# Kernel optimization log

Hardware: AMD Instinct MI355X
Metric: run time of the kernel (lower is better)

The kernel has to match this reference:

```python
import jax, jax.numpy as jnp
import numpy as np
from jax import lax

# ---- model dims (match init_kwargs) ----
D = 2048        # hidden_size
HD = 128        # head_dim
HQ = 16         # num_q_heads (= expanded_num_heads)
HK = 8          # num_k_heads = num_v_heads
CONV = 4        # conv_size
CHUNK = 64      # chunk_size
NUM_ITER = 30   # chebyshev iterations
RIDGE = 0.02
EPS = 1e-6


def setup_inputs() -> dict:
    key = jax.random.key(0)
    ks = jax.random.split(key, 20)
    s = 0.02
    inp = {}
    inp['hidden_states'] = jax.random.normal(ks[0], (1, 1024, D), jnp.float32)
    inp['Wq'] = jax.random.normal(ks[1], (D, HQ * HD), jnp.float32) * s
    inp['Wk'] = jax.random.normal(ks[2], (D, HK * HD), jnp.float32) * s
    inp['Wv'] = jax.random.normal(ks[3], (D, HK * HD), jnp.float32) * s
    inp['conv_q'] = jax.random.normal(ks[4], (HQ * HD, CONV), jnp.float32) * 0.3
    inp['conv_k'] = jax.random.normal(ks[5], (HK * HD, CONV), jnp.float32) * 0.3
    inp['conv_v'] = jax.random.normal(ks[6], (HK * HD, CONV), jnp.float32) * 0.3
    inp['Wa'] = jax.random.normal(ks[7], (D, HQ), jnp.float32) * s
    # A_log = log(Uniform(0,16)) as in torch init
    inp['A_log'] = jnp.log(jax.random.uniform(ks[8], (HQ,), jnp.float32, 1e-3, 16.0))
    # dt_bias = inverse-softplus of dt ~ LogUniform(1e-3, 1e-1)
    dt = jnp.exp(jax.random.uniform(ks[9], (HQ,), jnp.float32) * (np.log(0.1) - np.log(0.001)) + np.log(0.001))
    dt = jnp.clip(dt, 1e-4, None)
    inp['dt_bias'] = dt + jnp.log(-jnp.expm1(-dt))
    inp['Wb'] = jax.random.normal(ks[10], (D, HQ), jnp.float32) * s
    inp['bb'] = jnp.zeros((HQ,), jnp.float32)
    inp['Walpha'] = jax.random.normal(ks[11], (D, HQ), jnp.float32) * s
    inp['balpha'] = jnp.zeros((HQ,), jnp.float32)
    inp['Wg'] = jax.random.normal(ks[12], (D, HQ * HD), jnp.float32) * s
    inp['norm_w'] = jnp.ones((HD,), jnp.float32)
    inp['Wo'] = jax.random.normal(ks[13], (HQ * HD, D), jnp.float32) * s
    return inp


def short_conv(x, w):
    # causal depthwise conv1d (kernel=CONV) + silu; x:[B,L,C], w:[C,K]
    K = w.shape[1]
    L = x.shape[1]
    xp = jnp.pad(x, ((0, 0), (K - 1, 0), (0, 0)))
    y = sum(xp[:, j:j + L, :] * w[:, j] for j in range(K))
    return jax.nn.silu(y)


def cheb_solve(A, b, lmin, lmax, num_iter):
    # Chebyshev semi-iteration for SPD A x = b, eigenvalue bounds [lmin, lmax].
    # A, b: [..., d, d]; lmin scalar; lmax: [..., 1, 1]
    theta = (lmax + lmin) / 2.0
    delta = (lmax - lmin) / 2.0
    sigma1 = theta / delta
    x = jnp.zeros_like(b)
    r = b
    rho = 1.0 / sigma1
    dvec = r / theta
    def body(carry, _):
        x, r, dvec, rho = carry
        x = x + dvec
        r = r - jnp.einsum('...de,...ef->...df', A, dvec)
        rho_n = 1.0 / (2.0 * sigma1 - rho)
        dvec = rho_n * rho * dvec + (2.0 * rho_n / delta) * r
        return (x, r, dvec, rho_n), None
    (x, _, _, _), _ = lax.scan(body, (x, r, dvec, rho), None, length=num_iter)
    return x


def reference(hidden_states, Wq, Wk, Wv, conv_q, conv_k, conv_v, Wa, A_log, dt_bias,
              Wb, bb, Walpha, balpha, Wg, norm_w, Wo):
    x = hidden_states
    B, L, _ = x.shape
    H, Hk, d, C = HQ, HK, HD, CHUNK
    Nc = L // C

    # projections + short causal convs with silu
    q = short_conv(x @ Wq, conv_q).reshape(B, L, H, d) * (d ** -0.5)  # gla rescale
    k = short_conv(x @ Wk, conv_k).reshape(B, L, Hk, d)
    v = short_conv(x @ Wv, conv_v).reshape(B, L, Hk, d)
    grp = H // Hk
    k = jnp.repeat(k, grp, axis=2)  # GQA expand: (h g) ordering
    v = jnp.repeat(v, grp, axis=2)

    # gates
    glog = -jnp.exp(A_log) * jax.nn.softplus(x @ Wa + dt_bias)   # [B,L,H], log forgetting gate <= 0
    beta = jax.nn.sigmoid(x @ Wb + bb)                           # [B,L,H]
    alpha = jax.nn.sigmoid(x @ Walpha + balpha)                  # [B,L,H]

    # chunk: [B,H,Nc,C,...]
    def ch(t):
        return t.reshape(B, Nc, C, H, -1).transpose(0, 3, 1, 2, 4)
    qc, kc, vc = ch(q), ch(k), ch(v)
    glc = glog.reshape(B, Nc, C, H).transpose(0, 3, 1, 2)   # [B,H,Nc,C]
    bc = beta.reshape(B, Nc, C, H).transpose(0, 3, 1, 2)

    cs = jnp.cumsum(glc, axis=-1)         # inclusive cumulative log-decay within chunk
    G = cs[..., -1]                        # total chunk decay [B,H,Nc]
    w_end = jnp.exp(G[..., None] - cs) * bc
    dHn = jnp.einsum('bhnc,bhncd,bhnce->bhnde', w_end, kc, kc)  # gram increment (forgetting_gate_kk)
    dBn = jnp.einsum('bhnc,bhncd,bhnce->bhnde', w_end, kc, vc)  # kv increment
    dg = jnp.exp(G)

    # inter-chunk state recurrence (scan over chunks)
    def step(carry, inp):
        Hs, Bs = carry
        g_n, dH_n, dB_n = inp
        out = (Hs, Bs)  # state at chunk START
        Hs = g_n[..., None, None] * Hs + dH_n
        Bs = g_n[..., None, None] * Bs + dB_n
        return (Hs, Bs), out
    init = (jnp.zeros((B, H, d, d), x.dtype), jnp.zeros((B, H, d, d), x.dtype))
    inputs = (dg.transpose(2, 0, 1), dHn.transpose(2, 0, 1, 3, 4), dBn.transpose(2, 0, 1, 3, 4))
    _, (H0, B0) = lax.scan(step, init, inputs)  # [Nc,B,H,d,d]

    # ridge-regularized Kalman solve per chunk via Chebyshev
    A = H0 + RIDGE * jnp.eye(d, dtype=x.dtype)
    lmax = jnp.trace(A, axis1=-2, axis2=-1)[..., None, None]  # trace >= lambda_max for SPD
    X = cheb_solve(A, B0, RIDGE, lmax, NUM_ITER)              # [Nc,B,H,d,d]
    Xc = X.transpose(1, 2, 0, 3, 4)                           # [B,H,Nc,d,d]

    # inter-chunk readout (through solved state)
    o_inter = jnp.exp(cs)[..., None] * jnp.einsum('bhncd,bhnde->bhnce', qc, Xc)
    # intra-chunk causal gated attention
    diff = cs[..., :, None] - cs[..., None, :]                # [B,H,Nc,C,C]
    mask = jnp.tril(jnp.ones((C, C), bool))
    dmat = jnp.exp(jnp.where(mask, diff, -1e30))
    scores = jnp.einsum('bhncd,bhnjd->bhncj', qc, kc) * dmat * bc[..., None, :]
    o_intra = jnp.einsum('bhncj,bhnjd->bhncd', scores, vc)

    o = (o_inter + o_intra).transpose(0, 2, 3, 1, 4).reshape(B, L, H, d)
    o = o + alpha[..., None] * v   # alpha connection (residual value path)

    # gated RMSNorm + output projection
    g_out = (x @ Wg).reshape(B, L, H, d)
    o = o * lax.rsqrt(jnp.mean(o * o, axis=-1, keepdims=True) + EPS) * norm_w
    o = o * jax.nn.silu(g_out)
    return o.reshape(B, L, H * d) @ Wo
```

## Files before the change

### kernel.cpp

```cpp
#include <hip/hip_runtime.h>
#include <math.h>


#define LSEQ 1024
#define DM   2048
#define NHQ  16
#define NHK  8
#define HDIM 128
#define NCH  16
#define CSZ  64

typedef __attribute__((ext_vector_type(8))) short short8;
typedef __attribute__((ext_vector_type(4))) float floatx4;

__device__ __forceinline__ unsigned short f2bf(float f) {
  unsigned int u = __float_as_uint(f);
  u += 0x7fffu + ((u >> 16) & 1u);
  return (unsigned short)(u >> 16);
}
__device__ __forceinline__ float bf2f(unsigned short u) {
  return __uint_as_float(((unsigned int)u) << 16);
}

__device__ __forceinline__ void tcast_body(
    const float* __restrict__ W, unsigned short* __restrict__ Wt,
    int K, int N, int bn, int bk, int tid, float* __restrict__ t) {
  int r = tid >> 5, c = tid & 31;
#pragma unroll
  for (int i = 0; i < 4; ++i)
    t[(r + i * 8) * 33 + c] = W[(size_t)(bk * 32 + r + i * 8) * N + bn * 32 + c];
  __syncthreads();
#pragma unroll
  for (int i = 0; i < 4; ++i)
    Wt[(size_t)(bn * 32 + r + i * 8) * K + bk * 32 + c] =
        f2bf(t[c * 33 + r + i * 8]);
}

__global__ __launch_bounds__(256) void prep_kernel(
    const float* __restrict__ x, const float* __restrict__ Wq,
    const float* __restrict__ Wk, const float* __restrict__ Wv,
    const float* __restrict__ Wg, unsigned short* __restrict__ xb16,
    unsigned short* __restrict__ WtAll) {
  __shared__ float t[32 * 33];
  int b = blockIdx.x, tid = threadIdx.x;
  if (b < 2048) {
    int i = b * 256 + tid;
    float4 v = ((const float4*)x)[i];
    ushort4 u;
    u.x = f2bf(v.x); u.y = f2bf(v.y); u.z = f2bf(v.z); u.w = f2bf(v.w);
    ((ushort4*)xb16)[i] = u;
  } else if (b < 6144) {
    int r = b - 2048;
    tcast_body(Wq, WtAll, 2048, 2048, r & 63, r >> 6, tid, t);
  } else if (b < 8192) {
    int r = b - 6144;
    tcast_body(Wk, WtAll + (size_t)2048 * 2048, 2048, 1024, r & 31, r >> 5, tid, t);
  } else if (b < 10240) {
    int r = b - 8192;
    tcast_body(Wv, WtAll + (size_t)3072 * 2048, 2048, 1024, r & 31, r >> 5, tid, t);
  } else {
    int r = b - 10240;
    tcast_body(Wg, WtAll + (size_t)4096 * 2048, 2048, 2048, r & 63, r >> 6, tid, t);
  }
}

__global__ __launch_bounds__(256) void gemm_bf16(
    const unsigned short* __restrict__ A, const unsigned short* __restrict__ Bt,
    float* __restrict__ C, int M, int N, int K) {
  __shared__ unsigned short As[128 * 72];
  __shared__ unsigned short Bs[64 * 72];
  int tid = threadIdx.x;
  int wave = tid >> 6, lane = tid & 63;
  int ln = lane & 15, hi = lane >> 4;
  int wm = wave & 1, wn = wave >> 1;
  int m0 = blockIdx.y * 128, n0 = blockIdx.x * 64;

  floatx4 acc[4][2];
#pragma unroll
  for (int mt = 0; mt < 4; ++mt)
#pragma unroll
    for (int nt = 0; nt < 2; ++nt) acc[mt][nt] = (floatx4)(0.f);

  for (int k0 = 0; k0 < K; k0 += 64) {
#pragma unroll
    for (int g = 0; g < 4; ++g) {
      int l = tid + g * 256;
      int m = l >> 3, go = l & 7;
      uint4 v = *(const uint4*)(A + (size_t)(m0 + m) * K + k0 + go * 8);
      *(uint4*)(As + m * 72 + go * 8) = v;
    }
#pragma unroll
    for (int g = 0; g < 2; ++g) {
      int l = tid + g * 256;
      int n = l >> 3, go = l & 7;
      uint4 v = *(const uint4*)(Bt + (size_t)(n0 + n) * K + k0 + go * 8);
      *(uint4*)(Bs + n * 72 + go * 8) = v;
    }
    __syncthreads();
#pragma unroll
    for (int kb = 0; kb < 2; ++kb) {
      short8 a[4], b[2];
#pragma unroll
      for (int mt = 0; mt < 4; ++mt)
        a[mt] = *(const short8*)(As + (wm * 64 + mt * 16 + ln) * 72 + kb * 32 + hi * 8);
#pragma unroll
      for (int nt = 0; nt < 2; ++nt)
        b[nt] = *(const short8*)(Bs + (wn * 32 + nt * 16 + ln) * 72 + kb * 32 + hi * 8);
#pragma unroll
      for (int mt = 0; mt < 4; ++mt)
#pragma unroll
        for (int nt = 0; nt < 2; ++nt)
          acc[mt][nt] = __builtin_amdgcn_mfma_f32_16x16x32_bf16(
              a[mt], b[nt], acc[mt][nt], 0, 0, 0);
    }
    __syncthreads();
  }
#pragma unroll
  for (int mt = 0; mt < 4; ++mt)
#pragma unroll
    for (int nt = 0; nt < 2; ++nt) {
      int col = n0 + wn * 32 + nt * 16 + ln;
      int rowb = m0 + wm * 64 + mt * 16 + hi * 4;
#pragma unroll
      for (int r = 0; r < 4; ++r)
        C[(size_t)(rowb + r) * N + col] = acc[mt][nt][r];
    }
}

__device__ __forceinline__ float conv_core(
    const float* __restrict__ xin, const float* __restrict__ w,
    int idx, int instride, int nch, float scale) {
  int t = idx / nch, ch = idx - t * nch;
  float acc = 0.f;
#pragma unroll
  for (int j = 0; j < 4; ++j) {
    int tt = t + j - 3;
    float xv = (tt >= 0) ? xin[(size_t)tt * instride + ch] : 0.f;
    acc = fmaf(xv, w[ch * 4 + j], acc);
  }
  return acc / (1.f + expf(-acc)) * scale;
}

__global__ __launch_bounds__(256) void conv_all(
    const float* __restrict__ xall, const float* __restrict__ convq,
    const float* __restrict__ convk, const float* __restrict__ convv,
    unsigned short* __restrict__ qs16, float* __restrict__ ks2,
    unsigned short* __restrict__ ks16, float* __restrict__ vs2) {
  int b = blockIdx.x, tid = threadIdx.x;
  if (b < 8192) {
    int idx = b * 256 + tid;
    qs16[idx] = f2bf(conv_core(xall, convq, idx, 6144, 2048,
                               0.08838834764831845f));
  } else if (b < 12288) {
    int idx = (b - 8192) * 256 + tid;
    float v = conv_core(xall + 2048, convk, idx, 6144, 1024, 1.0f);
    ks2[idx] = v;
    ks16[idx] = f2bf(v);
  } else {
    int idx = (b - 12288) * 256 + tid;
    vs2[idx] = conv_core(xall + 3072, convv, idx, 6144, 1024, 1.0f);
  }
}

__global__ __launch_bounds__(256) void vtr_kernel(
    const float* __restrict__ vs, unsigned short* __restrict__ vT16) {
  int b = blockIdx.x;
  __shared__ float t[64 * 132];
  int tid = threadIdx.x;
  size_t gbase = ((size_t)(b >> 3)) * 65536 + ((size_t)(b & 7)) * 128;
#pragma unroll
  for (int g = 0; g < 8; ++g) {
    int i = tid + g * 256;
    int c = i >> 5, e4 = i & 31;
    float4 v = *(const float4*)(vs + gbase + (size_t)c * 1024 + e4 * 4);
    t[c * 132 + e4 * 4 + 0] = v.x;
    t[c * 132 + e4 * 4 + 1] = v.y;
    t[c * 132 + e4 * 4 + 2] = v.z;
    t[c * 132 + e4 * 4 + 3] = v.w;
  }
  __syncthreads();
  int e = tid >> 1, half = tid & 1;
  size_t obase = ((size_t)b << 13) + (size_t)e * 64 + half * 32;
#pragma unroll
  for (int cc = 0; cc < 8; ++cc) {
    int c0 = half * 32 + cc * 4;
    ushort4 u;
    u.x = f2bf(t[(c0 + 0) * 132 + e]);
    u.y = f2bf(t[(c0 + 1) * 132 + e]);
    u.z = f2bf(t[(c0 + 2) * 132 + e]);
    u.w = f2bf(t[(c0 + 3) * 132 + e]);
    *(ushort4*)(vT16 + obase + cc * 4) = u;
  }
}

__global__ __launch_bounds__(256) void gates_fused(
    const float* __restrict__ x, const float* __restrict__ Wa,
    const float* __restrict__ Wb, const float* __restrict__ Wal,
    const float* __restrict__ A_log, const float* __restrict__ dtb,
    const float* __restrict__ bbv, const float* __restrict__ balv,
    float* __restrict__ glog, float* __restrict__ beta,
    float* __restrict__ alpha) {
  int t = blockIdx.x;
  __shared__ float xr[2048];
  __shared__ float part[256];
  int tid = threadIdx.x;
  for (int i = tid; i < 512; i += 256)
    ((float4*)xr)[i] = ((const float4*)(x + (size_t)t * 2048))[i];
  __syncthreads();
  int o = tid >> 2, p = tid & 3;
  float s = 0.f;
  if (o < 48) {
    const float* W = (o < 16) ? Wa : (o < 32) ? Wb : Wal;
    int h = o & 15;
    int k0 = p * 512;
    for (int k = k0; k < k0 + 512; ++k) s = fmaf(xr[k], W[k * 16 + h], s);
  }
  part[tid] = s;
  __syncthreads();
  if (o < 48 && p == 0) {
    float dot = part[tid] + part[tid + 1] + part[tid + 2] + part[tid + 3];
    int h = o & 15;
    if (o < 16) {
      float za = dot + dtb[h];
      float sp = fmaxf(za, 0.f) + log1pf(expf(-fabsf(za)));
      glog[t * 16 + h] = -expf(A_log[h]) * sp;
    } else if (o < 32) {
      beta[t * 16 + h] = 1.f / (1.f + expf(-(dot + bbv[h])));
    } else {
      alpha[t * 16 + h] = 1.f / (1.f + expf(-(dot + balv[h])));
    }
  }
}

__global__ __launch_bounds__(256) void cumsum_kernel(
    const float* __restrict__ glog, const float* __restrict__ beta,
    float* __restrict__ cs, float* __restrict__ wend) {
  int idx = threadIdx.x;
  int n = idx & 15;
  float acc = 0.f;
  for (int c = 0; c < CSZ; ++c) {
    acc += glog[(n * CSZ + c) * NHQ + (idx >> 4)];
    cs[idx * CSZ + c] = acc;
  }
  float G = acc;
  for (int c = 0; c < CSZ; ++c) {
    wend[idx * CSZ + c] =
        expf(G - cs[idx * CSZ + c]) * beta[(n * CSZ + c) * NHQ + (idx >> 4)];
  }
}

__global__ __launch_bounds__(256) void dhb_kernel(
    const float* __restrict__ ks, const float* __restrict__ vs,
    const float* __restrict__ wend, float* __restrict__ dH,
    float* __restrict__ dB) {
  int bid = blockIdx.x;
  int h = bid >> 4, n = bid & 15;
  int hk = h >> 1;
  __shared__ unsigned short skF[2][8192];
  __shared__ unsigned short svF[2][8192];
  int tid = threadIdx.x;

#pragma unroll
  for (int p = 0; p < 4; ++p) {
    int t2 = tid + p * 256;
    int c0 = (t2 >> 7) << 3;
    int e = t2 & 127;
    int base = ((e >> 4) * 2 + (c0 >> 5)) * 512 +
               ((c0 & 31) >> 3) * 128 + (e & 15) * 8;
    unsigned short kh[8], kl[8], vh[8], vl[8];
#pragma unroll
    for (int j = 0; j < 8; ++j) {
      int c = c0 + j;
      float s = sqrtf(wend[bid * 64 + c]);
      size_t g = (size_t)(n * 64 + c) * 1024 + hk * 128 + e;
      float kf = s * ks[g];
      float vf = s * vs[g];
      unsigned short khh = f2bf(kf);
      kh[j] = khh; kl[j] = f2bf(kf - bf2f(khh));
      unsigned short vhh = f2bf(vf);
      vh[j] = vhh; vl[j] = f2bf(vf - bf2f(vhh));
    }
    *(uint4*)(&skF[0][base]) = *(uint4*)kh;
    *(uint4*)(&skF[1][base]) = *(uint4*)kl;
    *(uint4*)(&svF[0][base]) = *(uint4*)vh;
    *(uint4*)(&svF[1][base]) = *(uint4*)vl;
  }
  __syncthreads();

  int w = tid >> 6, lane = tid & 63;
  int ln = lane & 15, hi = lane >> 4;

  short8 ah[2][2], al[2][2];
#pragma unroll
  for (int mti = 0; mti < 2; ++mti) {
    int mt = w * 2 + mti;
#pragma unroll
    for (int ct = 0; ct < 2; ++ct) {
      ah[mti][ct] = *(const short8*)(&skF[0][((mt * 2 + ct) * 64 + lane) * 8]);
      al[mti][ct] = *(const short8*)(&skF[1][((mt * 2 + ct) * 64 + lane) * 8]);
    }
  }

  size_t gb = (size_t)bid << 14;
#pragma unroll
  for (int which = 0; which < 2; ++which) {
    const unsigned short (*BF)[8192] = which ? svF : skF;
    float* outp = which ? dB : dH;
#pragma unroll
    for (int nt = 0; nt < 8; ++nt) {
      floatx4 a0 = (floatx4)(0.f), a1 = (floatx4)(0.f);
#pragma unroll
      for (int ct = 0; ct < 2; ++ct) {
        short8 bh = *(const short8*)(&BF[0][((nt * 2 + ct) * 64 + lane) * 8]);
        short8 bl = *(const short8*)(&BF[1][((nt * 2 + ct) * 64 + lane) * 8]);
        a0 = __builtin_amdgcn_mfma_f32_16x16x32_bf16(ah[0][ct], bh, a0, 0, 0, 0);
        a0 = __builtin_amdgcn_mfma_f32_16x16x32_bf16(ah[0][ct], bl, a0, 0, 0, 0);
        a0 = __builtin_amdgcn_mfma_f32_16x16x32_bf16(al[0][ct], bh, a0, 0, 0, 0);
        a1 = __builtin_amdgcn_mfma_f32_16x16x32_bf16(ah[1][ct], bh, a1, 0, 0, 0);
        a1 = __builtin_amdgcn_mfma_f32_16x16x32_bf16(ah[1][ct], bl, a1, 0, 0, 0);
        a1 = __builtin_amdgcn_mfma_f32_16x16x32_bf16(al[1][ct], bh, a1, 0, 0, 0);
      }
      int e = nt * 16 + ln;
#pragma unroll
      for (int rg = 0; rg < 4; ++rg) {
        int d0 = (w * 2 + 0) * 16 + hi * 4 + rg;
        int d1 = (w * 2 + 1) * 16 + hi * 4 + rg;
        outp[gb + (size_t)d0 * 128 + e] = a0[rg];
        outp[gb + (size_t)d1 * 128 + e] = a1[rg];
      }
    }
  }
}

__global__ __launch_bounds__(256) void scan_kernel(
    float* __restrict__ dH, float* __restrict__ dB,
    const float* __restrict__ cs) {
  int idx = blockIdx.x * 256 + threadIdx.x;
  int h = idx >> 14, de = idx & 16383;
  float Hs = 0.f, Bs = 0.f;
  bool diag = ((de % 129) == 0);
#pragma unroll 1
  for (int n = 0; n < NCH; ++n) {
    size_t off = ((size_t)(h * 16 + n) << 14) + de;
    float dh = dH[off], db = dB[off];
    dH[off] = diag ? (Hs + 0.02f) : Hs;
    dB[off] = Bs;
    float g = expf(cs[(h * 16 + n) * CSZ + (CSZ - 1)]);
    Hs = fmaf(g, Hs, dh);
    Bs = fmaf(g, Bs, db);
  }
}

__global__ __launch_bounds__(256) void afrag_kernel(
    float* __restrict__ Aall, float* __restrict__ traces) {
  int bid = blockIdx.x;
  float* Ag = Aall + ((size_t)bid << 14);
  __shared__ float As[16384];
  int tid = threadIdx.x;
  for (int i = tid; i < 4096; i += 256)
    ((float4*)As)[i] = ((const float4*)Ag)[i];
  __syncthreads();
  if (tid < 64) {
    float tv = As[tid * 129] + As[(tid + 64) * 129];
#pragma unroll
    for (int off = 32; off; off >>= 1) tv += __shfl_down(tv, off);
    if (tid == 0) traces[bid] = tv;
  }
  unsigned short* Ah = (unsigned short*)Ag;
  unsigned short* Al = Ah + 16384;
#pragma unroll
  for (int c8 = 0; c8 < 8; ++c8) {
    int s0 = tid * 64 + c8 * 8;
    int frag = s0 >> 9, mlane = (s0 >> 3) & 63;
    int m = ((frag >> 2) << 4) + (mlane & 15);
    int k = ((frag & 3) << 5) + ((mlane >> 4) << 3);
    unsigned short hi[8], lo[8];
#pragma unroll
    for (int j = 0; j < 8; ++j) {
      float a = As[m * 128 + k + j];
      unsigned short h = f2bf(a);
      hi[j] = h;
      lo[j] = f2bf(a - bf2f(h));
    }
    *(uint4*)(Ah + s0) = *(uint4*)hi;
    *(uint4*)(Al + s0) = *(uint4*)lo;
  }
}

__global__ __launch_bounds__(512) void cheb_kernel(
    const unsigned short* __restrict__ Afrag, const float* __restrict__ traces,
    float* __restrict__ Ball) {
  int bid = blockIdx.x;
  const unsigned short* __restrict__ Ah = Afrag + ((size_t)bid << 15);
  float* __restrict__ Bg = Ball + ((size_t)bid << 14);
  __shared__ unsigned short dT[2][16384];
  int tid = threadIdx.x;
  int w = tid >> 6, lane = tid & 63;
  int ln = lane & 15, q = lane >> 4;

  float lmax = traces[bid];
  const float lmin = 0.02f;
  float theta = 0.5f * (lmax + lmin);
  float delta = 0.5f * (lmax - lmin);
  float sigma1 = theta / delta;
  float rho = delta / theta;
  float invtheta = 1.f / theta;

  short8 afr[4][2];
#pragma unroll
  for (int kt = 0; kt < 4; ++kt) {
    afr[kt][0] = *(const short8*)(Ah + (((w * 4 + kt) * 64 + lane) << 3));
    afr[kt][1] = *(const short8*)(Ah + 16384 + (((w * 4 + kt) * 64 + lane) << 3));
  }

  int wrA = ((w >> 1) * 64 + (((w & 1) * 2 + (q >> 1)) * 16 + ln)) * 8 +
            ((q & 1) << 2);

  float xx[8][4], rr[8][4], dd[8][4];
#pragma unroll
  for (int nt = 0; nt < 8; ++nt) {
    int nn = nt * 16 + ln;
    ushort4 pack;
    unsigned short* pp = (unsigned short*)&pack;
#pragma unroll
    for (int rg = 0; rg < 4; ++rg) {
      float b = Bg[(w * 16 + q * 4 + rg) * 128 + nn];
      rr[nt][rg] = b;
      xx[nt][rg] = 0.f;
      unsigned short dq = f2bf(b * invtheta);
      dd[nt][rg] = bf2f(dq);
      pp[rg] = dq;
    }
    *(ushort4*)(&dT[0][nt * 2048 + wrA]) = pack;
  }
  __syncthreads();

#pragma unroll 1
  for (int it = 0; it < 30; ++it) {
    const unsigned short* dTr = dT[it & 1];
    unsigned short* dTw = dT[(it & 1) ^ 1];
    floatx4 acc[8];
#pragma unroll
    for (int nt = 0; nt < 8; ++nt) acc[nt] = (floatx4)(0.f);
#pragma unroll
    for (int kt = 0; kt < 4; ++kt) {
      short8 df[8];
#pragma unroll
      for (int nt = 0; nt < 8; ++nt)
        df[nt] = *(const short8*)(dTr + (((nt * 4 + kt) * 64 + lane) << 3));
#pragma unroll
      for (int nt = 0; nt < 8; ++nt) {
        acc[nt] = __builtin_amdgcn_mfma_f32_16x16x32_bf16(
            afr[kt][0], df[nt], acc[nt], 0, 0, 0);
        acc[nt] = __builtin_amdgcn_mfma_f32_16x16x32_bf16(
            afr[kt][1], df[nt], acc[nt], 0, 0, 0);
      }
    }
    float rho_n = 1.f / (2.f * sigma1 - rho);
    float c1s = rho_n * rho;
    float c2s = 2.f * rho_n / delta;
#pragma unroll
    for (int nt = 0; nt < 8; ++nt) {
      ushort4 pack;
      unsigned short* pp = (unsigned short*)&pack;
#pragma unroll
      for (int rg = 0; rg < 4; ++rg) {
        xx[nt][rg] += dd[nt][rg];
        rr[nt][rg] -= acc[nt][rg];
        float dn = fmaf(c1s, dd[nt][rg], c2s * rr[nt][rg]);
        unsigned short dq = f2bf(dn);
        dd[nt][rg] = bf2f(dq);
        pp[rg] = dq;
      }
      *(ushort4*)(&dTw[nt * 2048 + wrA]) = pack;
    }
    rho = rho_n;
    __syncthreads();
  }

  unsigned short* Xf = (unsigned short*)Bg;
#pragma unroll
  for (int nt = 0; nt < 8; ++nt) {
    ushort4 h4, l4;
    unsigned short* hp = (unsigned short*)&h4;
    unsigned short* lp = (unsigned short*)&l4;
#pragma unroll
    for (int rg = 0; rg < 4; ++rg) {
      float xv = xx[nt][rg];
      unsigned short h = f2bf(xv);
      hp[rg] = h;
      lp[rg] = f2bf(xv - bf2f(h));
    }
    size_t off = (size_t)nt * 2048 + wrA;
    *(ushort4*)(Xf + off) = h4;
    *(ushort4*)(Xf + 16384 + off) = l4;
  }
}

__global__ __launch_bounds__(256) void attn_kernel(
    const unsigned short* __restrict__ q16, const unsigned short* __restrict__ k16,
    const unsigned short* __restrict__ vT16, const unsigned short* __restrict__ Xf,
    const float* __restrict__ vs, const float* __restrict__ cs,
    const float* __restrict__ beta, const float* __restrict__ alpha,
    float* __restrict__ o) {
  int bid = blockIdx.x;
  int h = bid >> 4, n = bid & 15;
  int hk = h >> 1;
  __shared__ unsigned short qb[64 * 136];
  __shared__ unsigned short kb[64 * 136];
  __shared__ unsigned short Sb[64 * 72];
  __shared__ float csL[64], ecsL[64], betaL[64], alphaL[64];
  int tid = threadIdx.x;
  int w = tid >> 6, lane = tid & 63;
  int ln = lane & 15, hi = lane >> 4;

  {
    size_t qgb = (((size_t)(n * 64)) * 16 + h) * 128;
    size_t kgb = (((size_t)(n * 64)) * 8 + hk) * 128;
#pragma unroll
    for (int g = 0; g < 4; ++g) {
      int i = tid + g * 256;
      int c = i >> 4, ch = i & 15;
      *(uint4*)(qb + c * 136 + ch * 8) =
          *(const uint4*)(q16 + qgb + (size_t)c * 2048 + ch * 8);
      *(uint4*)(kb + c * 136 + ch * 8) =
          *(const uint4*)(k16 + kgb + (size_t)c * 1024 + ch * 8);
    }
    if (tid < 64) {
      float cv = cs[bid * 64 + tid];
      csL[tid] = cv;
      ecsL[tid] = expf(cv);
      betaL[tid] = beta[(n * 64 + tid) * 16 + h];
      alphaL[tid] = alpha[(n * 64 + tid) * 16 + h];
    }
  }
  __syncthreads();

  short8 aq[4];
#pragma unroll
  for (int dt = 0; dt < 4; ++dt)
    aq[dt] = *(const short8*)(qb + (w * 16 + ln) * 136 + dt * 32 + hi * 8);

  const unsigned short* Xb = Xf + ((size_t)bid << 15);
  floatx4 acc[8];
#pragma unroll
  for (int et = 0; et < 8; ++et) {
    floatx4 a = (floatx4)(0.f);
#pragma unroll
    for (int dt = 0; dt < 4; ++dt) {
      short8 xh = *(const short8*)(Xb + (et * 4 + dt) * 512 + lane * 8);
      short8 xl = *(const short8*)(Xb + 16384 + (et * 4 + dt) * 512 + lane * 8);
      a = __builtin_amdgcn_mfma_f32_16x16x32_bf16(aq[dt], xh, a, 0, 0, 0);
      a = __builtin_amdgcn_mfma_f32_16x16x32_bf16(aq[dt], xl, a, 0, 0, 0);
    }
    acc[et] = a;
  }
#pragma unroll
  for (int et = 0; et < 8; ++et)
#pragma unroll
    for (int rg = 0; rg < 4; ++rg)
      acc[et][rg] *= ecsL[w * 16 + hi * 4 + rg];

#pragma unroll
  for (int jt = 0; jt < 4; ++jt) {
    if (jt <= w) {
      floatx4 s = (floatx4)(0.f);
#pragma unroll
      for (int dt = 0; dt < 4; ++dt) {
        short8 bk = *(const short8*)(kb + (jt * 16 + ln) * 136 + dt * 32 + hi * 8);
        s = __builtin_amdgcn_mfma_f32_16x16x32_bf16(aq[dt], bk, s, 0, 0, 0);
      }
      int j = jt * 16 + ln;
      float csj = csL[j], bj = betaL[j];
#pragma unroll
      for (int rg = 0; rg < 4; ++rg) {
        int c = w * 16 + hi * 4 + rg;
        float v = (j <= c) ? s[rg] * expf(csL[c] - csj) * bj : 0.f;
        Sb[c * 72 + j] = f2bf(v);
      }
    } else {
#pragma unroll
      for (int rg = 0; rg < 4; ++rg)
        Sb[(w * 16 + hi * 4 + rg) * 72 + jt * 16 + ln] = 0;
    }
  }

  const unsigned short* vTb = vT16 + ((size_t)(n * 8 + hk) << 13);
#pragma unroll
  for (int et = 0; et < 8; ++et) {
#pragma unroll
    for (int kt = 0; kt < 2; ++kt) {
      short8 as = *(const short8*)(Sb + (w * 16 + ln) * 72 + kt * 32 + hi * 8);
      short8 bv = *(const short8*)(vTb + (et * 16 + ln) * 64 + kt * 32 + hi * 8);
      acc[et] = __builtin_amdgcn_mfma_f32_16x16x32_bf16(as, bv, acc[et], 0, 0, 0);
    }
  }

#pragma unroll
  for (int et = 0; et < 8; ++et) {
#pragma unroll
    for (int rg = 0; rg < 4; ++rg) {
      int c = w * 16 + hi * 4 + rg, e = et * 16 + ln;
      size_t oaddr = (((size_t)(n * 64 + c)) * 16 + h) * 128 + e;
      size_t vaddr = (((size_t)(n * 64 + c)) * 8 + hk) * 128 + e;
      o[oaddr] = acc[et][rg] + alphaL[c] * vs[vaddr];
    }
  }
}

__global__ __launch_bounds__(256) void rmso_kernel(
    const float* __restrict__ o, const float* __restrict__ xall,
    const float* __restrict__ norm_w, unsigned short* __restrict__ onorm,
    const float* __restrict__ Wo, unsigned short* __restrict__ WtWo) {
  __shared__ float t[32 * 33];
  int b = blockIdx.x, tid = threadIdx.x;
  if (b < 4096) {
    int wave = tid >> 6, lane = tid & 63;
    int row = b * 4 + wave;
    size_t base = (size_t)row * HDIM;
    size_t gbase = (size_t)(row >> 4) * 6144 + 4096 + (size_t)(row & 15) * HDIM;
    float v0 = o[base + lane], v1 = o[base + lane + 64];
    float ss = fmaf(v0, v0, v1 * v1);
#pragma unroll
    for (int off = 32; off; off >>= 1) ss += __shfl_down(ss, off);
    ss = __shfl(ss, 0);
    float rinv = rsqrtf(ss * (1.f / 128.f) + 1e-6f);
    float g0 = xall[gbase + lane], g1 = xall[gbase + lane + 64];
    float s0 = g0 / (1.f + expf(-g0));
    float s1 = g1 / (1.f + expf(-g1));
    onorm[base + lane]      = f2bf(v0 * rinv * norm_w[lane] * s0);
    onorm[base + lane + 64] = f2bf(v1 * rinv * norm_w[lane + 64] * s1);
  } else {
    int r = b - 4096;
    tcast_body(Wo, WtWo, 2048, 2048, r & 63, r >> 6, tid, t);
  }
}

extern "C" void kernel_launch(void* const* d_in, const int* in_sizes, int n_in,
                              void* d_out, int out_size, void* d_ws,
                              size_t ws_size, hipStream_t stream) {
  (void)in_sizes; (void)n_in; (void)out_size; (void)ws_size;
  const float* x      = (const float*)d_in[0];
  const float* Wq     = (const float*)d_in[1];
  const float* Wk     = (const float*)d_in[2];
  const float* Wv     = (const float*)d_in[3];
  const float* convq  = (const float*)d_in[4];
  const float* convk  = (const float*)d_in[5];
  const float* convv  = (const float*)d_in[6];
  const float* Wa     = (const float*)d_in[7];
  const float* A_log  = (const float*)d_in[8];
  const float* dtb    = (const float*)d_in[9];
  const float* Wb     = (const float*)d_in[10];
  const float* bbv    = (const float*)d_in[11];
  const float* Wal    = (const float*)d_in[12];
  const float* balv   = (const float*)d_in[13];
  const float* Wg     = (const float*)d_in[14];
  const float* norm_w = (const float*)d_in[15];
  const float* Wo     = (const float*)d_in[16];
  float* out = (float*)d_out;

  float* p = (float*)d_ws;
  float* xall  = p; p += 6291456;
  float* qslot = p; p += 2097152;
  float* ks2   = p; p += 1048576;
  float* vs2   = p; p += 1048576;
  float* ob    = p; p += 2097152;
  float* glog  = p; p += 16384;
  float* beta  = p; p += 16384;
  float* alpha = p; p += 16384;
  float* csb   = p; p += 16384;
  float* wend  = p; p += 16384;
  float* traces= p; p += 16384;
  float* dHn   = p; p += 4194304;
  float* dBn   = p; p += 4194304;
  unsigned short* xb16 = (unsigned short*)p; p += 1048576;

  unsigned short* qs16 = (unsigned short*)qslot;
  unsigned short* ks16 = qs16 + 2097152;
  unsigned short* vT16 = ks16 + 1048576;
  unsigned short* WtAll = (unsigned short*)dHn;
  unsigned short* WtWo  = (unsigned short*)ks2;
  unsigned short* onorm16 = xb16;

  dim3 blk(256);
  prep_kernel<<<14336, blk, 0, stream>>>(x, Wq, Wk, Wv, Wg, xb16, WtAll);
  gemm_bf16<<<dim3(96, 8), blk, 0, stream>>>(xb16, WtAll, xall, 1024, 6144, 2048);
  conv_all<<<16384, blk, 0, stream>>>(xall, convq, convk, convv,
                                      qs16, ks2, ks16, vs2);
  vtr_kernel<<<128, blk, 0, stream>>>(vs2, vT16);
  gates_fused<<<1024, blk, 0, stream>>>(x, Wa, Wb, Wal, A_log, dtb, bbv, balv,
                                        glog, beta, alpha);
  cumsum_kernel<<<1, blk, 0, stream>>>(glog, beta, csb, wend);
  dhb_kernel<<<256, blk, 0, stream>>>(ks2, vs2, wend, dHn, dBn);
  scan_kernel<<<1024, blk, 0, stream>>>(dHn, dBn, csb);
  afrag_kernel<<<256, blk, 0, stream>>>(dHn, traces);
  cheb_kernel<<<256, dim3(512), 0, stream>>>((unsigned short*)dHn, traces, dBn);
  attn_kernel<<<256, blk, 0, stream>>>(qs16, ks16, vT16, (unsigned short*)dBn,
                                       vs2, csb, beta, alpha, ob);
  rmso_kernel<<<8192, blk, 0, stream>>>(ob, xall, norm_w, onorm16, Wo, WtWo);
  gemm_bf16<<<dim3(32, 8), blk, 0, stream>>>(onorm16, WtWo, out, 1024, 2048, 2048);
}
```

Measured before the change: 439.4 us.

## Split Chebyshev solve across column blocks and fuse small kernels into neighbors

The Chebyshev kernel now splits each head/chunk solve into four independent 32-column blocks. This raises the grid from 256 to 1024 workgroups, cuts per-block register and LDS use, and adds an occupancy hint. The solution layout is interleaved by column block, and the attention kernel's reads of it are updated to match. Separately, the gates, cumsum and V-transpose kernels become extra blocks in the prep, conv and dhb kernels, which removes three launches and their serialization gaps. The trade-off is that each Chebyshev block reloads the full A fragments, and the fused kernels carry extra shared memory and branching.

```diff
diff --git a/kernel.cpp b/kernel.cpp
--- a/kernel.cpp
+++ b/kernel.cpp
@@ -40,8 +40,15 @@
     const float* __restrict__ x, const float* __restrict__ Wq,
     const float* __restrict__ Wk, const float* __restrict__ Wv,
     const float* __restrict__ Wg, unsigned short* __restrict__ xb16,
-    unsigned short* __restrict__ WtAll) {
+    unsigned short* __restrict__ WtAll,
+    const float* __restrict__ Wa, const float* __restrict__ Wbeta,
+    const float* __restrict__ Wal, const float* __restrict__ A_log,
+    const float* __restrict__ dtb, const float* __restrict__ bbv,
+    const float* __restrict__ balv, float* __restrict__ glog,
+    float* __restrict__ beta, float* __restrict__ alpha) {
   __shared__ float t[32 * 33];
+  __shared__ float xr[2048];
+  __shared__ float part[256];
   int b = blockIdx.x, tid = threadIdx.x;
   if (b < 2048) {
     int i = b * 256 + tid;
@@ -58,9 +65,37 @@
   } else if (b < 10240) {
     int r = b - 8192;
     tcast_body(Wv, WtAll + (size_t)3072 * 2048, 2048, 1024, r & 31, r >> 5, tid, t);
-  } else {
+  } else if (b < 14336) {
     int r = b - 10240;
     tcast_body(Wg, WtAll + (size_t)4096 * 2048, 2048, 2048, r & 63, r >> 6, tid, t);
+  } else {
+    int ts = b - 14336;
+    for (int i = tid; i < 512; i += 256)
+      ((float4*)xr)[i] = ((const float4*)(x + (size_t)ts * 2048))[i];
+    __syncthreads();
+    int o = tid >> 2, p = tid & 3;
+    float s = 0.f;
+    if (o < 48) {
+      const float* W = (o < 16) ? Wa : (o < 32) ? Wbeta : Wal;
+      int h = o & 15;
+      int k0 = p * 512;
+      for (int k = k0; k < k0 + 512; ++k) s = fmaf(xr[k], W[k * 16 + h], s);
+    }
+    part[tid] = s;
+    __syncthreads();
+    if (o < 48 && p == 0) {
+      float dot = part[tid] + part[tid + 1] + part[tid + 2] + part[tid + 3];
+      int h = o & 15;
+      if (o < 16) {
+        float za = dot + dtb[h];
+        float sp = fmaxf(za, 0.f) + log1pf(expf(-fabsf(za)));
+        glog[ts * 16 + h] = -expf(A_log[h]) * sp;
+      } else if (o < 32) {
+        beta[ts * 16 + h] = 1.f / (1.f + expf(-(dot + bbv[h])));
+      } else {
+        alpha[ts * 16 + h] = 1.f / (1.f + expf(-(dot + balv[h])));
+      }
+    }
   }
 }
 
@@ -145,7 +180,9 @@
     const float* __restrict__ xall, const float* __restrict__ convq,
     const float* __restrict__ convk, const float* __restrict__ convv,
     unsigned short* __restrict__ qs16, float* __restrict__ ks2,
-    unsigned short* __restrict__ ks16, float* __restrict__ vs2) {
+    unsigned short* __restrict__ ks16, float* __restrict__ vs2,
+    const float* __restrict__ glog, const float* __restrict__ beta,
+    float* __restrict__ cs, float* __restrict__ wend) {
   int b = blockIdx.x, tid = threadIdx.x;
   if (b < 8192) {
     int idx = b * 256 + tid;
@@ -156,109 +193,68 @@
     float v = conv_core(xall + 2048, convk, idx, 6144, 1024, 1.0f);
     ks2[idx] = v;
     ks16[idx] = f2bf(v);
-  } else {
+  } else if (b < 16384) {
     int idx = (b - 12288) * 256 + tid;
     vs2[idx] = conv_core(xall + 3072, convv, idx, 6144, 1024, 1.0f);
-  }
-}
-
-__global__ __launch_bounds__(256) void vtr_kernel(
-    const float* __restrict__ vs, unsigned short* __restrict__ vT16) {
-  int b = blockIdx.x;
-  __shared__ float t[64 * 132];
-  int tid = threadIdx.x;
-  size_t gbase = ((size_t)(b >> 3)) * 65536 + ((size_t)(b & 7)) * 128;
-#pragma unroll
-  for (int g = 0; g < 8; ++g) {
-    int i = tid + g * 256;
-    int c = i >> 5, e4 = i & 31;
-    float4 v = *(const float4*)(vs + gbase + (size_t)c * 1024 + e4 * 4);
-    t[c * 132 + e4 * 4 + 0] = v.x;
-    t[c * 132 + e4 * 4 + 1] = v.y;
-    t[c * 132 + e4 * 4 + 2] = v.z;
-    t[c * 132 + e4 * 4 + 3] = v.w;
-  }
-  __syncthreads();
-  int e = tid >> 1, half = tid & 1;
-  size_t obase = ((size_t)b << 13) + (size_t)e * 64 + half * 32;
-#pragma unroll
-  for (int cc = 0; cc < 8; ++cc) {
-    int c0 = half * 32 + cc * 4;
-    ushort4 u;
-    u.x = f2bf(t[(c0 + 0) * 132 + e]);
-    u.y = f2bf(t[(c0 + 1) * 132 + e]);
-    u.z = f2bf(t[(c0 + 2) * 132 + e]);
-    u.w = f2bf(t[(c0 + 3) * 132 + e]);
-    *(ushort4*)(vT16 + obase + cc * 4) = u;
-  }
-}
-
-__global__ __launch_bounds__(256) void gates_fused(
-    const float* __restrict__ x, const float* __restrict__ Wa,
-    const float* __restrict__ Wb, const float* __restrict__ Wal,
-    const float* __restrict__ A_log, const float* __restrict__ dtb,
-    const float* __restrict__ bbv, const float* __restrict__ balv,
-    float* __restrict__ glog, float* __restrict__ beta,
-    float* __restrict__ alpha) {
-  int t = blockIdx.x;
-  __shared__ float xr[2048];
-  __shared__ float part[256];
-  int tid = threadIdx.x;
-  for (int i = tid; i < 512; i += 256)
-    ((float4*)xr)[i] = ((const float4*)(x + (size_t)t * 2048))[i];
-  __syncthreads();
-  int o = tid >> 2, p = tid & 3;
-  float s = 0.f;
-  if (o < 48) {
-    const float* W = (o < 16) ? Wa : (o < 32) ? Wb : Wal;
-    int h = o & 15;
-    int k0 = p * 512;
-    for (int k = k0; k < k0 + 512; ++k) s = fmaf(xr[k], W[k * 16 + h], s);
-  }
-  part[tid] = s;
-  __syncthreads();
-  if (o < 48 && p == 0) {
-    float dot = part[tid] + part[tid + 1] + part[tid + 2] + part[tid + 3];
-    int h = o & 15;
-    if (o < 16) {
-      float za = dot + dtb[h];
-      float sp = fmaxf(za, 0.f) + log1pf(expf(-fabsf(za)));
-      glog[t * 16 + h] = -expf(A_log[h]) * sp;
-    } else if (o < 32) {
-      beta[t * 16 + h] = 1.f / (1.f + expf(-(dot + bbv[h])));
-    } else {
-      alpha[t * 16 + h] = 1.f / (1.f + expf(-(dot + balv[h])));
-    }
-  }
-}
-
-__global__ __launch_bounds__(256) void cumsum_kernel(
-    const float* __restrict__ glog, const float* __restrict__ beta,
-    float* __restrict__ cs, float* __restrict__ wend) {
-  int idx = threadIdx.x;
-  int n = idx & 15;
-  float acc = 0.f;
-  for (int c = 0; c < CSZ; ++c) {
-    acc += glog[(n * CSZ + c) * NHQ + (idx >> 4)];
-    cs[idx * CSZ + c] = acc;
-  }
-  float G = acc;
-  for (int c = 0; c < CSZ; ++c) {
-    wend[idx * CSZ + c] =
-        expf(G - cs[idx * CSZ + c]) * beta[(n * CSZ + c) * NHQ + (idx >> 4)];
+  } else {
+    int idx = tid;
+    int n = idx & 15;
+    float acc = 0.f;
+    for (int c = 0; c < CSZ; ++c) {
+      acc += glog[(n * CSZ + c) * NHQ + (idx >> 4)];
+      cs[idx * CSZ + c] = acc;
+    }
+    float G = acc;
+    for (int c = 0; c < CSZ; ++c) {
+      wend[idx * CSZ + c] =
+          expf(G - cs[idx * CSZ + c]) * beta[(n * CSZ + c) * NHQ + (idx >> 4)];
+    }
   }
 }
 
 __global__ __launch_bounds__(256) void dhb_kernel(
     const float* __restrict__ ks, const float* __restrict__ vs,
     const float* __restrict__ wend, float* __restrict__ dH,
-    float* __restrict__ dB) {
+    float* __restrict__ dB, unsigned short* __restrict__ vT16) {
+  __shared__ uint4 smem4[4096];
   int bid = blockIdx.x;
+  int tid = threadIdx.x;
+
+  if (bid >= 256) {
+    float* t = (float*)smem4;
+    int b = bid - 256;
+    size_t gbase = ((size_t)(b >> 3)) * 65536 + ((size_t)(b & 7)) * 128;
+#pragma unroll
+    for (int g = 0; g < 8; ++g) {
+      int i = tid + g * 256;
+      int c = i >> 5, e4 = i & 31;
+      float4 v = *(const float4*)(vs + gbase + (size_t)c * 1024 + e4 * 4);
+      t[c * 132 + e4 * 4 + 0] = v.x;
+      t[c * 132 + e4 * 4 + 1] = v.y;
+      t[c * 132 + e4 * 4 + 2] = v.z;
+      t[c * 132 + e4 * 4 + 3] = v.w;
+    }
+    __syncthreads();
+    int e = tid >> 1, half = tid & 1;
+    size_t obase = ((size_t)b << 13) + (size_t)e * 64 + half * 32;
+#pragma unroll
+    for (int cc = 0; cc < 8; ++cc) {
+      int c0 = half * 32 + cc * 4;
+      ushort4 u;
+      u.x = f2bf(t[(c0 + 0) * 132 + e]);
+      u.y = f2bf(t[(c0 + 1) * 132 + e]);
+      u.z = f2bf(t[(c0 + 2) * 132 + e]);
+      u.w = f2bf(t[(c0 + 3) * 132 + e]);
+      *(ushort4*)(vT16 + obase + cc * 4) = u;
+    }
+    return;
+  }
+
+  unsigned short (*skF)[8192] = (unsigned short (*)[8192])smem4;
+  unsigned short (*svF)[8192] =
+      (unsigned short (*)[8192])((unsigned short*)smem4 + 16384);
   int h = bid >> 4, n = bid & 15;
   int hk = h >> 1;
-  __shared__ unsigned short skF[2][8192];
-  __shared__ unsigned short svF[2][8192];
-  int tid = threadIdx.x;
 
 #pragma unroll
   for (int p = 0; p < 4; ++p) {
@@ -387,18 +383,19 @@
   }
 }
 
-__global__ __launch_bounds__(512) void cheb_kernel(
+__global__ __launch_bounds__(512, 4) void cheb_kernel(
     const unsigned short* __restrict__ Afrag, const float* __restrict__ traces,
     float* __restrict__ Ball) {
-  int bid = blockIdx.x;
-  const unsigned short* __restrict__ Ah = Afrag + ((size_t)bid << 15);
-  float* __restrict__ Bg = Ball + ((size_t)bid << 14);
-  __shared__ unsigned short dT[2][16384];
+  int bm = blockIdx.x >> 2;
+  int cb = blockIdx.x & 3;
+  const unsigned short* __restrict__ Ah = Afrag + ((size_t)bm << 15);
+  float* __restrict__ Bg = Ball + ((size_t)bm << 14);
+  __shared__ unsigned short dT[2][4096];
   int tid = threadIdx.x;
   int w = tid >> 6, lane = tid & 63;
   int ln = lane & 15, q = lane >> 4;
 
-  float lmax = traces[bid];
+  float lmax = traces[bm];
   const float lmin = 0.02f;
   float theta = 0.5f * (lmax + lmin);
   float delta = 0.5f * (lmax - lmin);
@@ -416,10 +413,10 @@
   int wrA = ((w >> 1) * 64 + (((w & 1) * 2 + (q >> 1)) * 16 + ln)) * 8 +
             ((q & 1) << 2);
 
-  float xx[8][4], rr[8][4], dd[8][4];
-#pragma unroll
-  for (int nt = 0; nt < 8; ++nt) {
-    int nn = nt * 16 + ln;
+  float xx[2][4], rr[2][4], dd[2][4];
+#pragma unroll
+  for (int nt = 0; nt < 2; ++nt) {
+    int nn = cb * 32 + nt * 16 + ln;
     ushort4 pack;
     unsigned short* pp = (unsigned short*)&pack;
 #pragma unroll
@@ -439,28 +436,23 @@
   for (int it = 0; it < 30; ++it) {
     const unsigned short* dTr = dT[it & 1];
     unsigned short* dTw = dT[(it & 1) ^ 1];
-    floatx4 acc[8];
-#pragma unroll
-    for (int nt = 0; nt < 8; ++nt) acc[nt] = (floatx4)(0.f);
+    floatx4 acc[2];
+    acc[0] = (floatx4)(0.f);
+    acc[1] = (floatx4)(0.f);
 #pragma unroll
     for (int kt = 0; kt < 4; ++kt) {
-      short8 df[8];
-#pragma unroll
-      for (int nt = 0; nt < 8; ++nt)
-        df[nt] = *(const short8*)(dTr + (((nt * 4 + kt) * 64 + lane) << 3));
-#pragma unroll
-      for (int nt = 0; nt < 8; ++nt) {
-        acc[nt] = __builtin_amdgcn_mfma_f32_16x16x32_bf16(
-            afr[kt][0], df[nt], acc[nt], 0, 0, 0);
-        acc[nt] = __builtin_amdgcn_mfma_f32_16x16x32_bf16(
-            afr[kt][1], df[nt], acc[nt], 0, 0, 0);
-      }
+      short8 df0 = *(const short8*)(dTr + (((0 * 4 + kt) * 64 + lane) << 3));
+      short8 df1 = *(const short8*)(dTr + (((1 * 4 + kt) * 64 + lane) << 3));
+      acc[0] = __builtin_amdgcn_mfma_f32_16x16x32_bf16(afr[kt][0], df0, acc[0], 0, 0, 0);
+      acc[0] = __builtin_amdgcn_mfma_f32_16x16x32_bf16(afr[kt][1], df0, acc[0], 0, 0, 0);
+      acc[1] = __builtin_amdgcn_mfma_f32_16x16x32_bf16(afr[kt][0], df1, acc[1], 0, 0, 0);
+      acc[1] = __builtin_amdgcn_mfma_f32_16x16x32_bf16(afr[kt][1], df1, acc[1], 0, 0, 0);
     }
     float rho_n = 1.f / (2.f * sigma1 - rho);
     float c1s = rho_n * rho;
     float c2s = 2.f * rho_n / delta;
 #pragma unroll
-    for (int nt = 0; nt < 8; ++nt) {
+    for (int nt = 0; nt < 2; ++nt) {
       ushort4 pack;
       unsigned short* pp = (unsigned short*)&pack;
 #pragma unroll
@@ -480,7 +472,7 @@
 
   unsigned short* Xf = (unsigned short*)Bg;
 #pragma unroll
-  for (int nt = 0; nt < 8; ++nt) {
+  for (int nt = 0; nt < 2; ++nt) {
     ushort4 h4, l4;
     unsigned short* hp = (unsigned short*)&h4;
     unsigned short* lp = (unsigned short*)&l4;
@@ -491,9 +483,10 @@
       hp[rg] = h;
       lp[rg] = f2bf(xv - bf2f(h));
     }
-    size_t off = (size_t)nt * 2048 + wrA;
-    *(ushort4*)(Xf + off) = h4;
-    *(ushort4*)(Xf + 16384 + off) = l4;
+    int lhi = nt * 2048 + wrA;
+    int llo = lhi + 4096;
+    *(ushort4*)(Xf + ((lhi >> 6) * 256 + cb * 64 + (lhi & 63))) = h4;
+    *(ushort4*)(Xf + ((llo >> 6) * 256 + cb * 64 + (llo & 63))) = l4;
   }
 }
 
@@ -545,11 +538,14 @@
   floatx4 acc[8];
 #pragma unroll
   for (int et = 0; et < 8; ++et) {
+    int cbq = et >> 1, ntl = et & 1;
     floatx4 a = (floatx4)(0.f);
 #pragma unroll
     for (int dt = 0; dt < 4; ++dt) {
-      short8 xh = *(const short8*)(Xb + (et * 4 + dt) * 512 + lane * 8);
-      short8 xl = *(const short8*)(Xb + 16384 + (et * 4 + dt) * 512 + lane * 8);
+      int lhi = ntl * 2048 + dt * 512 + lane * 8;
+      int llo = lhi + 4096;
+      short8 xh = *(const short8*)(Xb + ((lhi >> 6) * 256 + cbq * 64 + (lhi & 63)));
+      short8 xl = *(const short8*)(Xb + ((llo >> 6) * 256 + cbq * 64 + (llo & 63)));
       a = __builtin_amdgcn_mfma_f32_16x16x32_bf16(aq[dt], xh, a, 0, 0, 0);
       a = __builtin_amdgcn_mfma_f32_16x16x32_bf16(aq[dt], xl, a, 0, 0, 0);
     }
@@ -683,18 +679,17 @@
   unsigned short* onorm16 = xb16;
 
   dim3 blk(256);
-  prep_kernel<<<14336, blk, 0, stream>>>(x, Wq, Wk, Wv, Wg, xb16, WtAll);
+  prep_kernel<<<15360, blk, 0, stream>>>(x, Wq, Wk, Wv, Wg, xb16, WtAll,
+                                         Wa, Wb, Wal, A_log, dtb, bbv, balv,
+                                         glog, beta, alpha);
   gemm_bf16<<<dim3(96, 8), blk, 0, stream>>>(xb16, WtAll, xall, 1024, 6144, 2048);
-  conv_all<<<16384, blk, 0, stream>>>(xall, convq, convk, convv,
-                                      qs16, ks2, ks16, vs2);
-  vtr_kernel<<<128, blk, 0, stream>>>(vs2, vT16);
-  gates_fused<<<1024, blk, 0, stream>>>(x, Wa, Wb, Wal, A_log, dtb, bbv, balv,
-                                        glog, beta, alpha);
-  cumsum_kernel<<<1, blk, 0, stream>>>(glog, beta, csb, wend);
-  dhb_kernel<<<256, blk, 0, stream>>>(ks2, vs2, wend, dHn, dBn);
+  conv_all<<<16385, blk, 0, stream>>>(xall, convq, convk, convv,
+                                      qs16, ks2, ks16, vs2,
+                                      glog, beta, csb, wend);
+  dhb_kernel<<<384, blk, 0, stream>>>(ks2, vs2, wend, dHn, dBn, vT16);
   scan_kernel<<<1024, blk, 0, stream>>>(dHn, dBn, csb);
   afrag_kernel<<<256, blk, 0, stream>>>(dHn, traces);
-  cheb_kernel<<<256, dim3(512), 0, stream>>>((unsigned short*)dHn, traces, dBn);
+  cheb_kernel<<<1024, dim3(512), 0, stream>>>((unsigned short*)dHn, traces, dBn);
   attn_kernel<<<256, blk, 0, stream>>>(qs16, ks16, vT16, (unsigned short*)dBn,
                                        vs2, csb, beta, alpha, ob);
   rmso_kernel<<<8192, blk, 0, stream>>>(ob, xall, norm_w, onorm16, Wo, WtWo);
```

New measurement: 445.2 us. About the same (+1.3%).
